# Kernel tuning notes

Hardware: AMD Instinct MI355X
Metric: run time of the kernel (lower is better)

Reference implementation:

```python
import jax, jax.numpy as jnp
import numpy as np


def setup_inputs() -> dict:
    key = jax.random.key(0)
    k1, k2, k3, k4 = jax.random.split(key, 4)
    B, S, E, H, V = 32, 4096, 512, 1024, 50257
    return {
        "decoder_hidden_s_t_1": jax.random.normal(k1, (B, H), dtype=jnp.float32),
        "mems": jax.random.randint(k2, (B, S), 0, V, dtype=jnp.int64),
        "emb_table": jax.random.normal(k3, (V, E), dtype=jnp.float32) * 0.02,
        "W_w": jax.random.normal(k4, (E, H), dtype=jnp.float32) * (1.0 / np.sqrt(H)),
        "W_b": jnp.zeros((E,), dtype=jnp.float32),
    }


def reference(decoder_hidden_s_t_1, mems, emb_table, W_w, W_b):
    # First-call path: build step_mem_embeddings from the memory token ids.
    # mems: [B, S] int -> mems_emb: [B, S, E]  (dropout is identity in eval)
    mems_emb = emb_table[mems]
    # v_t = tanh(W @ h + b): [B, E]
    v_t = jnp.tanh(decoder_hidden_s_t_1 @ W_w.T + W_b)
    # attention scores over memory slots: [B, S]
    scores = jnp.einsum("bse,be->bs", mems_emb, v_t)
    q_t = jax.nn.softmax(scores, axis=1)
    # weighted memory read: [B, 1, E]
    m_t = jnp.einsum("bs,bse->be", q_t, mems_emb)[:, None, :]
    return m_t
```

## Files before the change

### kernel.cpp

```cpp
#include <hip/hip_runtime.h>
#include <cmath>

#define B_ 32
#define S_ 4096
#define E_ 512
#define H_ 1024
#define NCHUNK 64

__global__ __launch_bounds__(256) void vt_kernel(const float* __restrict__ h,
                                                 const float* __restrict__ W,
                                                 const float* __restrict__ bias,
                                                 float* __restrict__ vt) {
    int wid  = threadIdx.x >> 6;
    int lane = threadIdx.x & 63;
    int out  = blockIdx.x * 4 + wid;
    int b    = out >> 9;
    int e    = out & (E_ - 1);
    const float* hrow = h + b * H_;
    const float* wrow = W + (size_t)e * H_;
    int base = lane * 16;
    float acc = 0.f;
#pragma unroll
    for (int j = 0; j < 4; ++j) {
        float4 hv = *reinterpret_cast<const float4*>(hrow + base + j * 4);
        float4 wv = *reinterpret_cast<const float4*>(wrow + base + j * 4);
        acc += hv.x * wv.x + hv.y * wv.y + hv.z * wv.z + hv.w * wv.w;
    }
#pragma unroll
    for (int off = 32; off > 0; off >>= 1) acc += __shfl_xor(acc, off, 64);
    if (lane == 0) vt[out] = tanhf(acc + bias[e]);
}

#define LOADG(IDX, pa0, pb0, pa1, pb1, pa2, pb2, pa3, pb3)                 \
    {                                                                      \
        const float* _r0 = emb + (size_t)(IDX).x * E_ + off8;              \
        const float* _r1 = emb + (size_t)(IDX).y * E_ + off8;              \
        const float* _r2 = emb + (size_t)(IDX).z * E_ + off8;              \
        const float* _r3 = emb + (size_t)(IDX).w * E_ + off8;              \
        pa0 = *reinterpret_cast<const float4*>(_r0);                       \
        pb0 = *reinterpret_cast<const float4*>(_r0 + 4);                   \
        pa1 = *reinterpret_cast<const float4*>(_r1);                       \
        pb1 = *reinterpret_cast<const float4*>(_r1 + 4);                   \
        pa2 = *reinterpret_cast<const float4*>(_r2);                       \
        pb2 = *reinterpret_cast<const float4*>(_r2 + 4);                   \
        pa3 = *reinterpret_cast<const float4*>(_r3);                       \
        pb3 = *reinterpret_cast<const float4*>(_r3 + 4);                   \
    }

#define PROC(a0, b0, a1, b1, a2, b2, a3, b3)                               \
    {                                                                      \
        float p0 = a0.x*v0.x + a0.y*v0.y + a0.z*v0.z + a0.w*v0.w          \
                 + b0.x*v1.x + b0.y*v1.y + b0.z*v1.z + b0.w*v1.w;         \
        float p1 = a1.x*v0.x + a1.y*v0.y + a1.z*v0.z + a1.w*v0.w          \
                 + b1.x*v1.x + b1.y*v1.y + b1.z*v1.z + b1.w*v1.w;         \
        float p2 = a2.x*v0.x + a2.y*v0.y + a2.z*v0.z + a2.w*v0.w          \
                 + b2.x*v1.x + b2.y*v1.y + b2.z*v1.z + b2.w*v1.w;         \
        float p3 = a3.x*v0.x + a3.y*v0.y + a3.z*v0.z + a3.w*v0.w          \
                 + b3.x*v1.x + b3.y*v1.y + b3.z*v1.z + b3.w*v1.w;         \
        _Pragma("unroll")                                                  \
        for (int off = 32; off > 0; off >>= 1) {                           \
            p0 += __shfl_xor(p0, off, 64);                                 \
            p1 += __shfl_xor(p1, off, 64);                                 \
            p2 += __shfl_xor(p2, off, 64);                                 \
            p3 += __shfl_xor(p3, off, 64);                                 \
        }                                                                  \
        float pm    = fmaxf(fmaxf(p0, p1), fmaxf(p2, p3));                 \
        float m_new = fmaxf(m, pm);                                        \
        float corr  = __expf(m - m_new);                                   \
        float w0 = __expf(p0 - m_new);                                     \
        float w1 = __expf(p1 - m_new);                                     \
        float w2 = __expf(p2 - m_new);                                     \
        float w3 = __expf(p3 - m_new);                                     \
        l = l * corr + (w0 + w1) + (w2 + w3);                              \
        acc0.x = acc0.x * corr + w0*a0.x + w1*a1.x + w2*a2.x + w3*a3.x;    \
        acc0.y = acc0.y * corr + w0*a0.y + w1*a1.y + w2*a2.y + w3*a3.y;    \
        acc0.z = acc0.z * corr + w0*a0.z + w1*a1.z + w2*a2.z + w3*a3.z;    \
        acc0.w = acc0.w * corr + w0*a0.w + w1*a1.w + w2*a2.w + w3*a3.w;    \
        acc1.x = acc1.x * corr + w0*b0.x + w1*b1.x + w2*b2.x + w3*b3.x;    \
        acc1.y = acc1.y * corr + w0*b0.y + w1*b1.y + w2*b2.y + w3*b3.y;    \
        acc1.z = acc1.z * corr + w0*b0.z + w1*b1.z + w2*b2.z + w3*b3.z;    \
        acc1.w = acc1.w * corr + w0*b0.w + w1*b1.w + w2*b2.w + w3*b3.w;    \
        m = m_new;                                                         \
    }

__global__ __launch_bounds__(256) void attn_part_kernel(const int* __restrict__ mems,
                                                        const float* __restrict__ emb,
                                                        const float* __restrict__ vt,
                                                        float* __restrict__ partial,
                                                        int nchunk) {
    int b     = blockIdx.x / nchunk;
    int chunk = blockIdx.x % nchunk;
    int wid   = threadIdx.x >> 6;
    int lane  = threadIdx.x & 63;
    int rows_per_block = S_ / nchunk;
    int rows_per_wave  = rows_per_block / 4;
    int s0 = chunk * rows_per_block + wid * rows_per_wave;
    int off8 = lane * 8;

    const float* vrow = vt + (size_t)b * E_ + off8;
    float4 v0 = *reinterpret_cast<const float4*>(vrow);
    float4 v1 = *reinterpret_cast<const float4*>(vrow + 4);

    float m = -1e30f, l = 0.f;
    float4 acc0 = {0.f, 0.f, 0.f, 0.f};
    float4 acc1 = {0.f, 0.f, 0.f, 0.f};

    const int* midx = mems + (size_t)b * S_;

    int4 iA = *reinterpret_cast<const int4*>(midx + s0);
    int4 iB = *reinterpret_cast<const int4*>(midx + s0 + 4);
    int4 iC = *reinterpret_cast<const int4*>(midx + s0 + 8);
    int4 iD = *reinterpret_cast<const int4*>(midx + s0 + 12);

    float4 xa0, xb0, xa1, xb1, xa2, xb2, xa3, xb3;
    float4 ya0, yb0, ya1, yb1, ya2, yb2, ya3, yb3;

    LOADG(iA, xa0, xb0, xa1, xb1, xa2, xb2, xa3, xb3);
    LOADG(iB, ya0, yb0, ya1, yb1, ya2, yb2, ya3, yb3);
    PROC(xa0, xb0, xa1, xb1, xa2, xb2, xa3, xb3);
    LOADG(iC, xa0, xb0, xa1, xb1, xa2, xb2, xa3, xb3);
    PROC(ya0, yb0, ya1, yb1, ya2, yb2, ya3, yb3);
    LOADG(iD, ya0, yb0, ya1, yb1, ya2, yb2, ya3, yb3);
    PROC(xa0, xb0, xa1, xb1, xa2, xb2, xa3, xb3);
    PROC(ya0, yb0, ya1, yb1, ya2, yb2, ya3, yb3);

    __shared__ float s_m[4], s_l[4];
    __shared__ float s_acc[4][E_];
    if (lane == 0) { s_m[wid] = m; s_l[wid] = l; }
    float* dst = &s_acc[wid][off8];
    reinterpret_cast<float4*>(dst)[0] = acc0;
    reinterpret_cast<float4*>(dst)[1] = acc1;
    __syncthreads();

    float mb = fmaxf(fmaxf(s_m[0], s_m[1]), fmaxf(s_m[2], s_m[3]));
    float f0 = __expf(s_m[0] - mb);
    float f1 = __expf(s_m[1] - mb);
    float f2 = __expf(s_m[2] - mb);
    float f3 = __expf(s_m[3] - mb);
    float lb = s_l[0] * f0 + s_l[1] * f1 + s_l[2] * f2 + s_l[3] * f3;

    float* base = partial + (size_t)(b * nchunk + chunk) * (E_ + 2);
    if (threadIdx.x == 0) { base[0] = mb; base[1] = lb; }
    for (int e = threadIdx.x; e < E_; e += 256) {
        base[2 + e] = s_acc[0][e] * f0 + s_acc[1][e] * f1
                    + s_acc[2][e] * f2 + s_acc[3][e] * f3;
    }
}

__global__ __launch_bounds__(512) void combine_kernel(const float* __restrict__ partial,
                                                      float* __restrict__ out,
                                                      int nchunk) {
    int b = blockIdx.x;
    int e = threadIdx.x;
    const int P = E_ + 2;
    const float* base = partial + (size_t)b * nchunk * P;
    float m_g = -1e30f;
    for (int c = 0; c < nchunk; ++c)
        m_g = fmaxf(m_g, base[(size_t)c * P]);
    float L = 0.f, s = 0.f;
    for (int c = 0; c < nchunk; ++c) {
        const float* p = base + (size_t)c * P;
        float f = __expf(p[0] - m_g);
        L += p[1] * f;
        s += f * p[2 + e];
    }
    out[(size_t)b * E_ + e] = s / L;
}

extern "C" void kernel_launch(void* const* d_in, const int* in_sizes, int n_in,
                              void* d_out, int out_size, void* d_ws, size_t ws_size,
                              hipStream_t stream) {
    const float* h    = (const float*)d_in[0];
    const int*   mems = (const int*)d_in[1];
    const float* emb  = (const float*)d_in[2];
    const float* W    = (const float*)d_in[3];
    const float* bias = (const float*)d_in[4];
    float* out = (float*)d_out;

    float* ws = (float*)d_ws;
    float* vt = ws;
    int nchunk = NCHUNK;
    while (nchunk > 1 &&
           (size_t)(B_ * E_ + B_ * nchunk * (E_ + 2)) * sizeof(float) > ws_size) {
        nchunk >>= 1;
    }
    float* partial = ws + B_ * E_;

    hipLaunchKernelGGL(vt_kernel, dim3(B_ * E_ / 4), dim3(256), 0, stream,
                       h, W, bias, vt);
    hipLaunchKernelGGL(attn_part_kernel, dim3(B_ * nchunk), dim3(256), 0, stream,
                       mems, emb, vt, partial, nchunk);
    hipLaunchKernelGGL(combine_kernel, dim3(B_), dim3(512), 0, stream,
                       partial, out, nchunk);
}
```

Measured before the change: 88.90 us.

## Sort memory token ids per batch row before gathering embeddings

```diff
diff --git a/kernel.cpp b/kernel.cpp
--- a/kernel.cpp
+++ b/kernel.cpp
@@ -29,6 +29,31 @@
 #pragma unroll
     for (int off = 32; off > 0; off >>= 1) acc += __shfl_xor(acc, off, 64);
     if (lane == 0) vt[out] = tanhf(acc + bias[e]);
+}
+
+__global__ __launch_bounds__(512) void sort_kernel(const int* __restrict__ mems,
+                                                   int* __restrict__ sorted) {
+    __shared__ int sh[S_];
+    int b = blockIdx.x;
+    const int* src = mems + (size_t)b * S_;
+    for (int i = threadIdx.x; i < S_; i += 512) sh[i] = src[i];
+    __syncthreads();
+    for (int k = 2; k <= S_; k <<= 1) {
+        for (int j = k >> 1; j > 0; j >>= 1) {
+            for (int i = threadIdx.x; i < S_; i += 512) {
+                int l = i ^ j;
+                if (l > i) {
+                    int a  = sh[i];
+                    int bb = sh[l];
+                    bool up = ((i & k) == 0);
+                    if (up ? (a > bb) : (a < bb)) { sh[i] = bb; sh[l] = a; }
+                }
+            }
+            __syncthreads();
+        }
+    }
+    int* dst = sorted + (size_t)b * S_;
+    for (int i = threadIdx.x; i < S_; i += 512) dst[i] = sh[i];
 }
 
 #define LOADG(IDX, pa0, pb0, pa1, pb1, pa2, pb2, pa3, pb3)                 \
@@ -83,13 +108,13 @@
         m = m_new;                                                         \
     }
 
-__global__ __launch_bounds__(256) void attn_part_kernel(const int* __restrict__ mems,
+__global__ __launch_bounds__(256) void attn_part_kernel(const int* __restrict__ sorted,
                                                         const float* __restrict__ emb,
                                                         const float* __restrict__ vt,
                                                         float* __restrict__ partial,
                                                         int nchunk) {
-    int b     = blockIdx.x / nchunk;
-    int chunk = blockIdx.x % nchunk;
+    int b     = blockIdx.x & (B_ - 1);
+    int chunk = blockIdx.x >> 5;
     int wid   = threadIdx.x >> 6;
     int lane  = threadIdx.x & 63;
     int rows_per_block = S_ / nchunk;
@@ -105,7 +130,7 @@
     float4 acc0 = {0.f, 0.f, 0.f, 0.f};
     float4 acc1 = {0.f, 0.f, 0.f, 0.f};
 
-    const int* midx = mems + (size_t)b * S_;
+    const int* midx = sorted + (size_t)b * S_;
 
     int4 iA = *reinterpret_cast<const int4*>(midx + s0);
     int4 iB = *reinterpret_cast<const int4*>(midx + s0 + 4);
@@ -179,17 +204,16 @@
 
     float* ws = (float*)d_ws;
     float* vt = ws;
+    int*   sorted = (int*)(ws + B_ * E_);
+    float* partial = ws + B_ * E_ + B_ * S_;
     int nchunk = NCHUNK;
-    while (nchunk > 1 &&
-           (size_t)(B_ * E_ + B_ * nchunk * (E_ + 2)) * sizeof(float) > ws_size) {
-        nchunk >>= 1;
-    }
-    float* partial = ws + B_ * E_;
 
     hipLaunchKernelGGL(vt_kernel, dim3(B_ * E_ / 4), dim3(256), 0, stream,
                        h, W, bias, vt);
+    hipLaunchKernelGGL(sort_kernel, dim3(B_), dim3(512), 0, stream,
+                       mems, sorted);
     hipLaunchKernelGGL(attn_part_kernel, dim3(B_ * nchunk), dim3(256), 0, stream,
-                       mems, emb, vt, partial, nchunk);
+                       sorted, emb, vt, partial, nchunk);
     hipLaunchKernelGGL(combine_kernel, dim3(B_), dim3(512), 0, stream,
                        partial, out, nchunk);
 }
```

Result: slower. 177.5 us (+99.7%).
